# Kernel tuning notes

Hardware: AMD Instinct MI355X
Metric: run time of the kernel (lower is better)

## Reference

```python
import jax, jax.numpy as jnp
import numpy as np

B, H, K, D = 4096, 512, 32, 20


def setup_inputs() -> dict:
    key = jax.random.key(0)
    k1, k2 = jax.random.split(key)
    hidden = jax.random.normal(k1, (B, H), dtype=jnp.float32)
    # cluster: soft assignment probabilities (rows sum to 1), like a softmax output
    c = jax.random.uniform(k2, (B, K), dtype=jnp.float32)
    cluster = c / jnp.sum(c, axis=-1, keepdims=True)
    return {"hidden": hidden, "cluster": cluster, "d": D}


def reference(hidden, cluster, d):
    # softHidden[b,h,k] = hidden[b,h] * cluster[b,k]
    soft_hidden = hidden[:, :, None] * cluster[:, None, :]          # [B,H,K]
    class_sums = jnp.sum(soft_hidden, axis=0)                        # [H,K] (code calls these "class_means" but they are sums)
    within = jnp.sum((soft_hidden - class_sums[None]) ** 2, axis=0)  # [H,K]
    # round() has zero gradient in torch; mirror that with stop_gradient
    counts = jax.lax.stop_gradient(jnp.round(jnp.sum(cluster, axis=0)))  # [K]

    m = class_sums.T   # [K,H]
    w = within.T       # [K,H]

    # all class pairs i<j (the nested Python loops, vectorized)
    i, j = jnp.triu_indices(K, k=1)   # each [P], P = K*(K-1)/2
    mi, mj = m[i], m[j]                               # [P,H]
    gm = (mi + mj) / 2.0
    between = (mi - gm) ** 2 * counts[i][:, None] + (mj - gm) ** 2 * counts[j][:, None]
    pair_within = w[i] + w[j]                         # [P,H]
    pair_count = counts[i] + counts[j]                # [P]

    d2 = pair_count - 2.0
    d2 = jnp.where(d2 == 0.0, d2 + 1e-5, d2)
    x = between / (between + pair_within)
    x = jnp.clip(x, 1e-37, 1.0 - 1e-5)
    # regularized incomplete beta I_x(d1/2, d2/2) with d1 = 1
    xbetainc = jax.scipy.special.betainc(0.5, (d2 / 2.0)[:, None], x)  # [P,H]

    top_k, _ = jax.lax.top_k(xbetainc, d)             # [P,d]
    per_pair = jnp.sum(jnp.log(top_k), axis=-1)       # [P]
    return -jnp.sum(per_pair)
```

## Files before the change

kernel.cpp:

```cpp
#include <hip/hip_runtime.h>
#include <math.h>

#define BB 4096
#define HH 512
#define KK 32
#define PAIRS ((KK * (KK - 1)) / 2)

constexpr int TH  = 16;
constexpr int NBB = 16;
constexpr int BC  = BB / NBB;
constexpr int SUB = 64;

__global__ __launch_bounds__(256) void stage1_kernel(
    const float* __restrict__ hidden, const float* __restrict__ cluster,
    float* __restrict__ msum, float* __restrict__ s2sum,
    float* __restrict__ colsum)
{
    __shared__ float hid_s [SUB * TH];
    __shared__ float clu_s [SUB * KK];
    __shared__ float red   [8 * TH * KK];

    const int t  = threadIdx.x;
    const int ty = t >> 5;
    const int tx = t & 31;
    const int h0 = blockIdx.x * TH;
    const int bchunk = blockIdx.y * BC;

    float acc_m[TH], acc_s[TH];
#pragma unroll
    for (int i = 0; i < TH; ++i) { acc_m[i] = 0.f; acc_s[i] = 0.f; }
    float csum = 0.f;

    const float4* hid4 = (const float4*)hidden;
    const float4* clu4 = (const float4*)cluster;

    for (int sub = 0; sub < BC; sub += SUB) {
        const int b0 = bchunk + sub;
        {
            int r = t >> 2, q = t & 3;
            ((float4*)hid_s)[t] =
                hid4[(size_t)(b0 + r) * (HH / 4) + (h0 >> 2) + q];
        }
#pragma unroll
        for (int e = 0; e < 2; ++e) {
            int u = t + e * 256;
            int r = u >> 3, q = u & 7;
            ((float4*)clu_s)[u] = clu4[(size_t)(b0 + r) * (KK / 4) + q];
        }
        __syncthreads();

#pragma unroll
        for (int s = 0; s < SUB / 8; ++s) {
            int r = s * 8 + ty;
            float c  = clu_s[r * KK + tx];
            float c2 = c * c;
            csum += c;
#pragma unroll
            for (int hh = 0; hh < TH; ++hh) {
                float hv = hid_s[r * TH + hh];
                acc_m[hh] = fmaf(hv,      c,  acc_m[hh]);
                acc_s[hh] = fmaf(hv * hv, c2, acc_s[hh]);
            }
        }
        __syncthreads();
    }

    if (blockIdx.x == 0) atomicAdd(&colsum[tx], csum);

#pragma unroll
    for (int hh = 0; hh < TH; ++hh) red[ty * (TH * KK) + hh * KK + tx] = acc_m[hh];
    __syncthreads();
    for (int u = t; u < TH * KK; u += 256) {
        float v = 0.f;
#pragma unroll
        for (int g = 0; g < 8; ++g) v += red[g * (TH * KK) + u];
        int hh = u >> 5, k = u & 31;
        atomicAdd(&msum[(size_t)k * HH + h0 + hh], v);
    }
    __syncthreads();
#pragma unroll
    for (int hh = 0; hh < TH; ++hh) red[ty * (TH * KK) + hh * KK + tx] = acc_s[hh];
    __syncthreads();
    for (int u = t; u < TH * KK; u += 256) {
        float v = 0.f;
#pragma unroll
        for (int g = 0; g < 8; ++g) v += red[g * (TH * KK) + u];
        int hh = u >> 5, k = u & 31;
        atomicAdd(&s2sum[(size_t)k * HH + h0 + hh], v);
    }
}

__device__ __forceinline__ float frcp(float x) {
#if __has_builtin(__builtin_amdgcn_rcpf)
    return __builtin_amdgcn_rcpf(x);
#else
    return 1.0f / x;
#endif
}
__device__ __forceinline__ float guardf(float t) {
    return (fabsf(t) < 1e-30f) ? 1e-30f : t;
}

__device__ float betacf_fast(float a, float b, float x)
{
    const float EPS = 1e-5f;
    float qab = a + b, qap = a + 1.0f, qam = a - 1.0f;
    float c = 1.0f;
    float d = frcp(guardf(1.0f - qab * x * frcp(qap)));
    float h = d;
    for (int m = 1; m <= 100; ++m) {
        float fm = (float)m, m2 = 2.0f * fm;
        float aa = fm * (b - fm) * x * frcp((qam + m2) * (a + m2));
        d = frcp(guardf(fmaf(aa, d, 1.0f)));
        c = guardf(fmaf(aa, frcp(c), 1.0f));
        h *= d * c;
        float aa2 = -(a + fm) * (qab + fm) * x * frcp((a + m2) * (qap + m2));
        d = frcp(guardf(fmaf(aa2, d, 1.0f)));
        c = guardf(fmaf(aa2, frcp(c), 1.0f));
        float del = d * c;
        h *= del;
        if (__all(fabsf(del - 1.0f) < EPS)) break;
    }
    return h;
}

__global__ __launch_bounds__(64) void stage2_kernel(
    const float* __restrict__ msum, const float* __restrict__ s2sum,
    const float* __restrict__ colsum, const int* __restrict__ dptr,
    float* __restrict__ out)
{
    const int lane = threadIdx.x;
    const int p = blockIdx.x;

    int i = 0, rem = p;
    while (true) { int row = KK - 1 - i; if (rem < row) break; rem -= row; ++i; }
    const int j = i + 1 + rem;

    const float ci = roundf(colsum[i]);
    const float cj = roundf(colsum[j]);
    const float pc = ci + cj;
    float d2 = pc - 2.0f;
    if (d2 == 0.0f) d2 = 1e-5f;
    const float a = 0.5f;
    const float b = 0.5f * d2;
    const float lg = lgammaf(a + b) - lgammaf(b) - 0.57236494f;
    const float xsplit = (a + 1.0f) / (a + b + 2.0f);

    const float* mi_p = msum  + (size_t)i * HH;
    const float* mj_p = msum  + (size_t)j * HH;
    const float* si_p = s2sum + (size_t)i * HH;
    const float* sj_p = s2sum + (size_t)j * HH;

    float lv[8];
#pragma unroll
    for (int q = 0; q < 8; ++q) {
        int h = q * 64 + lane;
        float mi = mi_p[h], mj = mj_p[h];
        float wi = fmaf((float)(BB - 2) * mi, mi, si_p[h]);
        float wj = fmaf((float)(BB - 2) * mj, mj, sj_p[h]);
        float dm = 0.5f * (mi - mj);
        float between = dm * dm * pc;
        float denom = between + wi + wj;
        float x = between / denom;
        if (!(x >= 1e-37f)) x = 1e-37f;
        x = fminf(x, 1.0f - 1e-5f);
        lv[q] = x;
    }

    const int d = *dptr;

    float myx = 0.004f;
    float lm = lv[0];
#pragma unroll
    for (int q = 1; q < 8; ++q) lm = fmaxf(lm, lv[q]);

    for (int r = 0; r < d; ++r) {
        float gm = lm;
#pragma unroll
        for (int off = 1; off < 64; off <<= 1)
            gm = fmaxf(gm, __shfl_xor(gm, off));
        unsigned long long msk = __ballot(lm == gm);
        int winner = __ffsll((unsigned long long)msk) - 1;
        if (lane == r) myx = gm;
        if (lane == winner) {
            bool done = false;
#pragma unroll
            for (int q = 0; q < 8; ++q)
                if (!done && lv[q] == gm) { lv[q] = -1.0f; done = true; }
            lm = lv[0];
#pragma unroll
            for (int q = 1; q < 8; ++q) lm = fmaxf(lm, lv[q]);
        }
    }

    float x   = myx;
    float omx = 1.0f - x;
    bool  brA = x < xsplit;
    float al  = brA ? a : b;
    float be  = brA ? b : a;
    float xx  = brA ? x : omx;
    float cf  = betacf_fast(al, be, xx);
    float lbt = lg + 0.5f * logf(x) + b * logf(omx);
    float L;
    if (brA) {
        L = lbt + logf(2.0f * fmaxf(cf, 1e-30f));
    } else {
        float tt = expf(lbt) * cf / b;
        tt = fminf(tt, 0.99999988f);
        L = log1pf(-tt);
    }

    float val = (lane < d) ? L : 0.0f;
#pragma unroll
    for (int off = 1; off < 64; off <<= 1) val += __shfl_xor(val, off);
    if (lane == 0) atomicAdd(out, -val);
}

extern "C" void kernel_launch(void* const* d_in, const int* in_sizes, int n_in,
                              void* d_out, int out_size, void* d_ws, size_t ws_size,
                              hipStream_t stream)
{
    const float* hidden  = (const float*)d_in[0];
    const float* cluster = (const float*)d_in[1];
    const int*   dptr    = (const int*)d_in[2];

    float* msum   = (float*)d_ws;
    float* s2sum  = msum + HH * KK;
    float* colsum = s2sum + HH * KK;

    size_t zbytes = (size_t)(2 * HH * KK + KK) * sizeof(float);
    hipMemsetAsync(d_ws, 0, zbytes, stream);
    hipMemsetAsync(d_out, 0, sizeof(float), stream);

    dim3 g1(HH / TH, NBB);
    stage1_kernel<<<g1, 256, 0, stream>>>(hidden, cluster, msum, s2sum, colsum);
    stage2_kernel<<<PAIRS, 64, 0, stream>>>(msum, s2sum, colsum, dptr,
                                            (float*)d_out);
}
```

Before: 102.8 us.

## Replace atomic accumulation and memsets with per-chunk partials and last-block finalize

Stage 1 now writes per-batch-chunk partial sums of the class sums, squared sums and column sums to separate workspace slots, with padded shared-memory reduction. This replaces global atomics and removes the two memset launches. Stage 2 uses 256 threads to reduce the 16 partials per pair and stage the x values through shared memory. A counter-based last-block pattern writes the final output in place of a pre-zeroed output. The trade-off is that each pair block now reads 16x more partial data, and the control slots are reset inside stage 1, which depends on launch ordering.

```diff
diff --git a/kernel.cpp b/kernel.cpp
--- a/kernel.cpp
+++ b/kernel.cpp
@@ -10,21 +10,30 @@
 constexpr int NBB = 16;
 constexpr int BC  = BB / NBB;
 constexpr int SUB = 64;
+constexpr int RP  = TH + 1;
+
 
 __global__ __launch_bounds__(256) void stage1_kernel(
     const float* __restrict__ hidden, const float* __restrict__ cluster,
-    float* __restrict__ msum, float* __restrict__ s2sum,
-    float* __restrict__ colsum)
-{
-    __shared__ float hid_s [SUB * TH];
-    __shared__ float clu_s [SUB * KK];
-    __shared__ float red   [8 * TH * KK];
+    float* __restrict__ part_m, float* __restrict__ part_s,
+    float* __restrict__ pcol, float* __restrict__ ctl)
+{
+    __shared__ float hid_s[SUB * TH];
+    __shared__ float clu_s[SUB * KK];
+    __shared__ float red  [8 * KK * RP];
+    __shared__ float cred [8 * KK];
 
     const int t  = threadIdx.x;
     const int ty = t >> 5;
     const int tx = t & 31;
     const int h0 = blockIdx.x * TH;
-    const int bchunk = blockIdx.y * BC;
+    const int c  = blockIdx.y;
+    const int bchunk = c * BC;
+
+    if (blockIdx.x == 0 && c == 0 && t == 0) {
+        ctl[0] = 0.0f;
+        ((unsigned*)ctl)[1] = 0u;
+    }
 
     float acc_m[TH], acc_s[TH];
 #pragma unroll
@@ -52,41 +61,50 @@
 #pragma unroll
         for (int s = 0; s < SUB / 8; ++s) {
             int r = s * 8 + ty;
-            float c  = clu_s[r * KK + tx];
-            float c2 = c * c;
-            csum += c;
+            float cc = clu_s[r * KK + tx];
+            float c2 = cc * cc;
+            csum += cc;
 #pragma unroll
             for (int hh = 0; hh < TH; ++hh) {
                 float hv = hid_s[r * TH + hh];
-                acc_m[hh] = fmaf(hv,      c,  acc_m[hh]);
+                acc_m[hh] = fmaf(hv,      cc, acc_m[hh]);
                 acc_s[hh] = fmaf(hv * hv, c2, acc_s[hh]);
             }
         }
         __syncthreads();
     }
 
-    if (blockIdx.x == 0) atomicAdd(&colsum[tx], csum);
-
-#pragma unroll
-    for (int hh = 0; hh < TH; ++hh) red[ty * (TH * KK) + hh * KK + tx] = acc_m[hh];
-    __syncthreads();
-    for (int u = t; u < TH * KK; u += 256) {
+    cred[ty * KK + tx] = csum;
+    __syncthreads();
+    if (blockIdx.x == 0 && t < KK) {
         float v = 0.f;
 #pragma unroll
-        for (int g = 0; g < 8; ++g) v += red[g * (TH * KK) + u];
-        int hh = u >> 5, k = u & 31;
-        atomicAdd(&msum[(size_t)k * HH + h0 + hh], v);
-    }
-    __syncthreads();
-#pragma unroll
-    for (int hh = 0; hh < TH; ++hh) red[ty * (TH * KK) + hh * KK + tx] = acc_s[hh];
-    __syncthreads();
-    for (int u = t; u < TH * KK; u += 256) {
+        for (int g = 0; g < 8; ++g) v += cred[g * KK + t];
+        pcol[c * KK + t] = v;
+    }
+
+#pragma unroll
+    for (int hh = 0; hh < TH; ++hh)
+        red[ty * (KK * RP) + tx * RP + hh] = acc_m[hh];
+    __syncthreads();
+    for (int u = t; u < KK * TH; u += 256) {
+        int k = u >> 4, hh = u & 15;
         float v = 0.f;
 #pragma unroll
-        for (int g = 0; g < 8; ++g) v += red[g * (TH * KK) + u];
-        int hh = u >> 5, k = u & 31;
-        atomicAdd(&s2sum[(size_t)k * HH + h0 + hh], v);
+        for (int g = 0; g < 8; ++g) v += red[g * (KK * RP) + k * RP + hh];
+        part_m[((size_t)c * KK + k) * HH + h0 + hh] = v;
+    }
+    __syncthreads();
+#pragma unroll
+    for (int hh = 0; hh < TH; ++hh)
+        red[ty * (KK * RP) + tx * RP + hh] = acc_s[hh];
+    __syncthreads();
+    for (int u = t; u < KK * TH; u += 256) {
+        int k = u >> 4, hh = u & 15;
+        float v = 0.f;
+#pragma unroll
+        for (int g = 0; g < 8; ++g) v += red[g * (KK * RP) + k * RP + hh];
+        part_s[((size_t)c * KK + k) * HH + h0 + hh] = v;
     }
 }
 
@@ -124,50 +142,66 @@
     return h;
 }
 
-__global__ __launch_bounds__(64) void stage2_kernel(
-    const float* __restrict__ msum, const float* __restrict__ s2sum,
-    const float* __restrict__ colsum, const int* __restrict__ dptr,
-    float* __restrict__ out)
-{
-    const int lane = threadIdx.x;
+__global__ __launch_bounds__(256) void stage2_kernel(
+    const float* __restrict__ part_m, const float* __restrict__ part_s,
+    const float* __restrict__ pcol, float* __restrict__ ctl,
+    const int* __restrict__ dptr, float* __restrict__ out)
+{
+    __shared__ float xs[HH];
+
+    const int t = threadIdx.x;
+    const int w = t >> 6, lane = t & 63;
     const int p = blockIdx.x;
 
     int i = 0, rem = p;
     while (true) { int row = KK - 1 - i; if (rem < row) break; rem -= row; ++i; }
     const int j = i + 1 + rem;
 
-    const float ci = roundf(colsum[i]);
-    const float cj = roundf(colsum[j]);
+    float ci = 0.f, cj = 0.f;
+#pragma unroll
+    for (int cc = 0; cc < NBB; ++cc) {
+        ci += pcol[cc * KK + i];
+        cj += pcol[cc * KK + j];
+    }
+    ci = roundf(ci); cj = roundf(cj);
     const float pc = ci + cj;
     float d2 = pc - 2.0f;
     if (d2 == 0.0f) d2 = 1e-5f;
     const float a = 0.5f;
     const float b = 0.5f * d2;
-    const float lg = lgammaf(a + b) - lgammaf(b) - 0.57236494f;
-    const float xsplit = (a + 1.0f) / (a + b + 2.0f);
-
-    const float* mi_p = msum  + (size_t)i * HH;
-    const float* mj_p = msum  + (size_t)j * HH;
-    const float* si_p = s2sum + (size_t)i * HH;
-    const float* sj_p = s2sum + (size_t)j * HH;
-
-    float lv[8];
-#pragma unroll
-    for (int q = 0; q < 8; ++q) {
-        int h = q * 64 + lane;
-        float mi = mi_p[h], mj = mj_p[h];
-        float wi = fmaf((float)(BB - 2) * mi, mi, si_p[h]);
-        float wj = fmaf((float)(BB - 2) * mj, mj, sj_p[h]);
+
+#pragma unroll
+    for (int q = 0; q < 2; ++q) {
+        int h = w * 128 + q * 64 + lane;
+        float mi = 0.f, mj = 0.f, si = 0.f, sj = 0.f;
+#pragma unroll
+        for (int cc = 0; cc < NBB; ++cc) {
+            size_t base = (size_t)cc * KK * HH;
+            mi += part_m[base + (size_t)i * HH + h];
+            mj += part_m[base + (size_t)j * HH + h];
+            si += part_s[base + (size_t)i * HH + h];
+            sj += part_s[base + (size_t)j * HH + h];
+        }
+        float wi = fmaf((float)(BB - 2) * mi, mi, si);
+        float wj = fmaf((float)(BB - 2) * mj, mj, sj);
         float dm = 0.5f * (mi - mj);
         float between = dm * dm * pc;
         float denom = between + wi + wj;
         float x = between / denom;
         if (!(x >= 1e-37f)) x = 1e-37f;
         x = fminf(x, 1.0f - 1e-5f);
-        lv[q] = x;
-    }
+        xs[h] = x;
+    }
+    __syncthreads();
+    if (w != 0) return;
+
+    float lv[8];
+#pragma unroll
+    for (int q = 0; q < 8; ++q) lv[q] = xs[q * 64 + lane];
 
     const int d = *dptr;
+    const float lg = lgammaf(a + b) - lgammaf(b) - 0.57236494f;
+    const float xsplit = (a + 1.0f) / (a + b + 2.0f);
 
     float myx = 0.004f;
     float lm = lv[0];
@@ -213,7 +247,15 @@
     float val = (lane < d) ? L : 0.0f;
 #pragma unroll
     for (int off = 1; off < 64; off <<= 1) val += __shfl_xor(val, off);
-    if (lane == 0) atomicAdd(out, -val);
+
+    if (lane == 0) {
+        atomicAdd(&ctl[0], -val);
+        __threadfence();
+        unsigned old = atomicAdd((unsigned*)ctl + 1, 1u);
+        if (old == PAIRS - 1) {
+            out[0] = atomicAdd(&ctl[0], 0.0f);
+        }
+    }
 }
 
 extern "C" void kernel_launch(void* const* d_in, const int* in_sizes, int n_in,
@@ -224,16 +266,14 @@
     const float* cluster = (const float*)d_in[1];
     const int*   dptr    = (const int*)d_in[2];
 
-    float* msum   = (float*)d_ws;
-    float* s2sum  = msum + HH * KK;
-    float* colsum = s2sum + HH * KK;
-
-    size_t zbytes = (size_t)(2 * HH * KK + KK) * sizeof(float);
-    hipMemsetAsync(d_ws, 0, zbytes, stream);
-    hipMemsetAsync(d_out, 0, sizeof(float), stream);
+    float* part_m = (float*)d_ws;
+    float* part_s = part_m + (size_t)NBB * KK * HH;
+    float* pcol   = part_s + (size_t)NBB * KK * HH;
+    float* ctl    = pcol + NBB * KK;
 
     dim3 g1(HH / TH, NBB);
-    stage1_kernel<<<g1, 256, 0, stream>>>(hidden, cluster, msum, s2sum, colsum);
-    stage2_kernel<<<PAIRS, 64, 0, stream>>>(msum, s2sum, colsum, dptr,
-                                            (float*)d_out);
-}
+    stage1_kernel<<<g1, 256, 0, stream>>>(hidden, cluster,
+                                          part_m, part_s, pcol, ctl);
+    stage2_kernel<<<PAIRS, 256, 0, stream>>>(part_m, part_s, pcol, ctl,
+                                             dptr, (float*)d_out);
+}
```

Result: faster. 95.35 us (-7.2%).
